# Optimization experiments

Measured on AMD Instinct MI355X. Metric: run time of the kernel, lower is better.

Reference implementation:

```python
import jax, jax.numpy as jnp
import numpy as np

IN_FEATURES = 4096
OUT_FEATURES = 1024
BATCH = 16384
WERR = 1.0
BERR = 1.0


def setup_inputs() -> dict:
    key = jax.random.key(0)
    kx, kw = jax.random.split(key)
    X = jax.random.normal(kx, (BATCH, IN_FEATURES), dtype=jnp.float32)
    # glorot_uniform init for W, zeros for bias (as in Keras layer)
    limit = np.sqrt(6.0 / (IN_FEATURES + OUT_FEATURES)).astype(np.float32)
    W = jax.random.uniform(kw, (IN_FEATURES, OUT_FEATURES), dtype=jnp.float32,
                           minval=-limit, maxval=limit)
    bias = jnp.zeros((1, OUT_FEATURES), dtype=jnp.float32)
    return {"X": X, "W": W, "bias": bias}


def reference(X, W, bias):
    # Binarize weights/bias with sign(), scaled by Werr/Berr, then dense matmul.
    Wb = jnp.sign(W) * WERR          # [in, out], values in {-1, 0, +1}
    bb = jnp.sign(bias) * BERR       # [1, out]
    Z = jnp.matmul(X, Wb) + bb       # [batch, out]
    return Z
```

## Files before the change

### kernel.cpp

```cpp
#include <hip/hip_runtime.h>

#define M_DIM 16384
#define N_DIM 1024
#define K_DIM 4096

#define BM 256
#define BN 256
#define BK 64
#define NT (K_DIM / BK)

typedef __attribute__((ext_vector_type(4))) float f32x4;
typedef __attribute__((ext_vector_type(8))) short bf16x8;
typedef __attribute__((ext_vector_type(8))) unsigned short u16x8;

static __device__ __forceinline__ short f2bf(float f) {
  union { __bf16 h; short s; } u;
  u.h = (__bf16)f;
  return u.s;
}

static __device__ __forceinline__ void load_lds16(const void* g, void* l) {
  __builtin_amdgcn_global_load_lds(
      (const __attribute__((address_space(1))) void*)g,
      (__attribute__((address_space(3))) void*)l, 16, 0, 0);
}

__global__ __launch_bounds__(256) void wsign_transpose(
    const float* __restrict__ W, unsigned short* __restrict__ WbT) {
  __shared__ unsigned short tile[64][72];
  const int t  = (int)threadIdx.x;
  const int k0 = (int)(blockIdx.x >> 4) * 64;
  const int n0 = (int)(blockIdx.x & 15) * 64;
#pragma unroll
  for (int p = 0; p < 4; ++p) {
    const int r = p * 16 + (t >> 4);
    const int c = (t & 15) * 4;
    const float* src = W + (size_t)(k0 + r) * N_DIM + n0 + c;
#pragma unroll
    for (int j = 0; j < 4; ++j) {
      const float w = src[j];
      tile[r][c + j] = (w > 0.f) ? (unsigned short)0x3F80u
                                 : ((w < 0.f) ? (unsigned short)0xBF80u
                                              : (unsigned short)0u);
    }
  }
  __syncthreads();
  const int n  = t >> 2;
  const int kg = (t & 3) * 16;
  u16x8 o0, o1;
#pragma unroll
  for (int j = 0; j < 8; ++j) o0[j] = tile[kg + j][n];
#pragma unroll
  for (int j = 0; j < 8; ++j) o1[j] = tile[kg + 8 + j][n];
  unsigned short* dst = WbT + (size_t)(n0 + n) * K_DIM + k0 + kg;
  *(u16x8*)dst       = o0;
  *(u16x8*)(dst + 8) = o1;
}

__global__ __launch_bounds__(512, 2) void gemm_p4(
    const float* __restrict__ X, const unsigned short* __restrict__ WbT,
    const float* __restrict__ bias, float* __restrict__ Z) {
  __shared__ __align__(16) unsigned short As[2][BM * BK];
  __shared__ __align__(16) unsigned short Bs[2][BN * BK];

  const int t   = (int)threadIdx.x;
  const int l   = t & 63;
  const int wid = t >> 6;
  const int wm  = wid >> 2;
  const int wn  = wid & 3;

  const int bid = (int)blockIdx.x;
  const int swz = (bid & 7) * 32 + (bid >> 3);
  const int m0  = (swz >> 2) * BM;
  const int n0  = (swz & 3) * BN;

  const int abase = (wm * 128 + (l & 15)) * BK;
  const int bbase = (wn * 64 + (l & 15)) * BK;
  const int axk0  = (((l >> 4) + 0) ^ (l & 7)) << 3;
  const int axk1  = (((l >> 4) + 4) ^ (l & 7)) << 3;

  const float* sA0 = X + (size_t)(m0 +   0 + (t >> 3)) * K_DIM + (t & 7) * 8;
  const float* sA1 = X + (size_t)(m0 +  64 + (t >> 3)) * K_DIM + (t & 7) * 8;
  const float* sA2 = X + (size_t)(m0 + 128 + (t >> 3)) * K_DIM + (t & 7) * 8;
  const float* sA3 = X + (size_t)(m0 + 192 + (t >> 3)) * K_DIM + (t & 7) * 8;
  const int adst = (t >> 3) * BK + (((t & 7) ^ ((t >> 3) & 7)) << 3);

  const unsigned short* b_src[4];
  int b_dst[4];
#pragma unroll
  for (int i = 0; i < 4; ++i) {
    const int c = i * 512 + t;
    const int n = c >> 3, gp = c & 7;
    b_src[i] = WbT + (size_t)(n0 + n) * K_DIM + (gp ^ (n & 7)) * 8;
    b_dst[i] = c * 8;
  }

  f32x4 acc[8][4] = {};
  f32x4 ar1[2][2], ar2[2][2];
  bf16x8 aF[2][4];
  bf16x8 bF0[2][2], bF1[2][2];

#define SB0 __builtin_amdgcn_sched_barrier(0)
#define BAR do { SB0; __builtin_amdgcn_s_barrier(); SB0; } while (0)
#define WVM(N) do { asm volatile("s_waitcnt vmcnt(" #N ")" ::: "memory"); SB0; } while (0)
#define WLG0 do { asm volatile("s_waitcnt lgkmcnt(0)" ::: "memory"); SB0; } while (0)

#define LD_A1(KT)                                                          \
  do { SB0;                                                                \
    ar1[0][0] = *(const f32x4*)(sA0 + (KT));                               \
    ar1[0][1] = *(const f32x4*)(sA0 + (KT) + 4);                           \
    ar1[1][0] = *(const f32x4*)(sA1 + (KT));                               \
    ar1[1][1] = *(const f32x4*)(sA1 + (KT) + 4); SB0;                      \
  } while (0)
#define LD_A2(KT)                                                          \
  do { SB0;                                                                \
    ar2[0][0] = *(const f32x4*)(sA2 + (KT));                               \
    ar2[0][1] = *(const f32x4*)(sA2 + (KT) + 4);                           \
    ar2[1][0] = *(const f32x4*)(sA3 + (KT));                               \
    ar2[1][1] = *(const f32x4*)(sA3 + (KT) + 4); SB0;                      \
  } while (0)
#define WR_A(AR, BUF, OFS)                                                 \
  do {                                                                     \
    _Pragma("unroll") for (int j = 0; j < 2; ++j) {                        \
      u16x8 v;                                                             \
      _Pragma("unroll") for (int q = 0; q < 4; ++q) {                      \
        v[q]     = (unsigned short)f2bf(AR[j][0][q]);                      \
        v[4 + q] = (unsigned short)f2bf(AR[j][1][q]);                      \
      }                                                                    \
      *(u16x8*)(&As[BUF][adst + (OFS) + j * 4096]) = v;                    \
    }                                                                      \
  } while (0)
#define DMA_B2(KT, BUF, I0)                                                \
  do { SB0;                                                                \
    _Pragma("unroll") for (int i = (I0); i < (I0) + 2; ++i)                \
      load_lds16(b_src[i] + (KT), &Bs[BUF][b_dst[i]]);                     \
    SB0;                                                                   \
  } while (0)
#define RD_A(MH, AB)                                                       \
  do { SB0;                                                                \
    _Pragma("unroll") for (int mi = 0; mi < 4; ++mi) {                     \
      aF[0][mi] = *(const bf16x8*)((AB) + abase + ((MH)*4 + mi) * 1024 + axk0); \
      aF[1][mi] = *(const bf16x8*)((AB) + abase + ((MH)*4 + mi) * 1024 + axk1); \
    } SB0;                                                                 \
  } while (0)
#define RD_B(DST, NH, BB)                                                  \
  do { SB0;                                                                \
    _Pragma("unroll") for (int nj = 0; nj < 2; ++nj) {                     \
      DST[0][nj] = *(const bf16x8*)((BB) + bbase + ((NH)*2 + nj) * 1024 + axk0); \
      DST[1][nj] = *(const bf16x8*)((BB) + bbase + ((NH)*2 + nj) * 1024 + axk1); \
    } SB0;                                                                 \
  } while (0)
#define Q(MH, NH, BF)                                                      \
  do { __builtin_amdgcn_s_setprio(1);                                      \
    _Pragma("unroll") for (int kk = 0; kk < 2; ++kk)                       \
      _Pragma("unroll") for (int mi = 0; mi < 4; ++mi)                     \
        _Pragma("unroll") for (int nj = 0; nj < 2; ++nj)                   \
          acc[(MH)*4 + mi][(NH)*2 + nj] =                                  \
              __builtin_amdgcn_mfma_f32_16x16x32_bf16(                     \
                  aF[kk][mi], BF[kk][nj], acc[(MH)*4 + mi][(NH)*2 + nj],   \
                  0, 0, 0);                                                \
    __builtin_amdgcn_s_setprio(0);                                         \
  } while (0)

  LD_A1(0); LD_A2(0);
  WVM(4); WR_A(ar1, 0, 0);
  WVM(0); WR_A(ar2, 0, 8192);
  DMA_B2(0, 0, 0); DMA_B2(0, 0, 2);
  LD_A1(BK); LD_A2(BK);
  WLG0;
  BAR;

  for (int tt = 0; tt < NT - 2; ++tt) {
    const int cur = tt & 1, nxt = cur ^ 1;
    const unsigned short* Ab = As[cur];
    const unsigned short* Bb = Bs[cur];
    const int kt1 = (tt + 1) * BK, kt2 = (tt + 2) * BK;
    WVM(8);
    RD_A(0, Ab);
    RD_B(bF0, 0, Bb);
    BAR; WLG0;
    Q(0, 0, bF0);
    BAR;
    WVM(4);
    WR_A(ar1, nxt, 0);
    RD_B(bF1, 1, Bb);
    DMA_B2(kt1, nxt, 0);
    BAR; WLG0;
    Q(0, 1, bF1);
    BAR;
    WVM(2);
    WR_A(ar2, nxt, 8192);
    RD_A(1, Ab);
    DMA_B2(kt1, nxt, 2);
    LD_A1(kt2);
    BAR; WLG0;
    Q(1, 1, bF1);
    BAR;
    LD_A2(kt2);
    Q(1, 0, bF0);
    BAR;
  }

  {
    const int cur = (NT - 2) & 1, nxt = cur ^ 1;
    const unsigned short* Ab = As[cur];
    const unsigned short* Bb = Bs[cur];
    const int kt1 = (NT - 1) * BK;
    WVM(8);
    RD_A(0, Ab);
    RD_B(bF0, 0, Bb);
    BAR; WLG0;
    Q(0, 0, bF0);
    BAR;
    WVM(4);
    WR_A(ar1, nxt, 0);
    RD_B(bF1, 1, Bb);
    DMA_B2(kt1, nxt, 0);
    BAR; WLG0;
    Q(0, 1, bF1);
    BAR;
    WVM(2);
    WR_A(ar2, nxt, 8192);
    RD_A(1, Ab);
    DMA_B2(kt1, nxt, 2);
    BAR; WLG0;
    Q(1, 1, bF1);
    BAR;
    Q(1, 0, bF0);
    BAR;
  }
  {
    const unsigned short* Ab = As[(NT - 1) & 1];
    const unsigned short* Bb = Bs[(NT - 1) & 1];
    WVM(0);
    RD_A(0, Ab);
    RD_B(bF0, 0, Bb);
    WLG0;
    Q(0, 0, bF0);
    RD_B(bF1, 1, Bb);
    WLG0;
    Q(0, 1, bF1);
    RD_A(1, Ab);
    WLG0;
    Q(1, 1, bF1);
    Q(1, 0, bF0);
  }

#pragma unroll
  for (int ni = 0; ni < 4; ++ni) {
    const int col = n0 + wn * 64 + ni * 16 + (l & 15);
    const float b  = bias[col];
    const float bs = (b > 0.f) ? 1.f : ((b < 0.f) ? -1.f : 0.f);
#pragma unroll
    for (int mi = 0; mi < 8; ++mi) {
      const int row = m0 + wm * 128 + mi * 16 + ((l >> 4) << 2);
#pragma unroll
      for (int j = 0; j < 4; ++j)
        Z[(size_t)(row + j) * N_DIM + col] = acc[mi][ni][j] + bs;
    }
  }
#undef SB0
#undef BAR
#undef WVM
#undef WLG0
#undef LD_A1
#undef LD_A2
#undef WR_A
#undef DMA_B2
#undef RD_A
#undef RD_B
#undef Q
}

__global__ __launch_bounds__(256) void naive_fb(
    const float* __restrict__ X, const float* __restrict__ W,
    const float* __restrict__ bias, float* __restrict__ Z) {
  const size_t id = (size_t)blockIdx.x * 256 + threadIdx.x;
  const int m = (int)(id >> 10), n = (int)(id & 1023);
  float acc = 0.f;
  for (int k = 0; k < K_DIM; ++k) {
    const float w = W[(size_t)k * N_DIM + n];
    const float s = (w > 0.f) ? 1.f : ((w < 0.f) ? -1.f : 0.f);
    acc += X[(size_t)m * K_DIM + k] * s;
  }
  const float b = bias[n];
  Z[id] = acc + ((b > 0.f) ? 1.f : ((b < 0.f) ? -1.f : 0.f));
}

extern "C" void kernel_launch(void* const* d_in, const int* in_sizes, int n_in,
                              void* d_out, int out_size, void* d_ws, size_t ws_size,
                              hipStream_t stream) {
  const float* X    = (const float*)d_in[0];
  const float* W    = (const float*)d_in[1];
  const float* bias = (const float*)d_in[2];
  float* Z = (float*)d_out;

  const size_t needW = (size_t)N_DIM * K_DIM * sizeof(unsigned short);
  if (ws_size >= needW) {
    unsigned short* WbT = (unsigned short*)d_ws;
    wsign_transpose<<<dim3((K_DIM / 64) * (N_DIM / 64)), dim3(256), 0, stream>>>(W, WbT);
    gemm_p4<<<dim3((M_DIM / BM) * (N_DIM / BN)), dim3(512), 0, stream>>>(X, WbT, bias, Z);
  } else {
    naive_fb<<<dim3((size_t)M_DIM * N_DIM / 256), dim3(256), 0, stream>>>(X, W, bias, Z);
  }
}
```

Before: 187.1 us.

## Restructure GEMM inner loop into k-slice phases with 4x4 MFMA blocks

```diff
diff --git a/kernel.cpp b/kernel.cpp
--- a/kernel.cpp
+++ b/kernel.cpp
@@ -57,7 +57,7 @@
   *(u16x8*)(dst + 8) = o1;
 }
 
-__global__ __launch_bounds__(512, 2) void gemm_p4(
+__global__ __launch_bounds__(512, 2) void gemm_kk(
     const float* __restrict__ X, const unsigned short* __restrict__ WbT,
     const float* __restrict__ bias, float* __restrict__ Z) {
   __shared__ __align__(16) unsigned short As[2][BM * BK];
@@ -96,38 +96,35 @@
   }
 
   f32x4 acc[8][4] = {};
-  f32x4 ar1[2][2], ar2[2][2];
-  bf16x8 aF[2][4];
-  bf16x8 bF0[2][2], bF1[2][2];
+  f32x4 ar[4][2];
+  bf16x8 aR[4];
+  bf16x8 bR[4];
 
 #define SB0 __builtin_amdgcn_sched_barrier(0)
 #define BAR do { SB0; __builtin_amdgcn_s_barrier(); SB0; } while (0)
 #define WVM(N) do { asm volatile("s_waitcnt vmcnt(" #N ")" ::: "memory"); SB0; } while (0)
 #define WLG0 do { asm volatile("s_waitcnt lgkmcnt(0)" ::: "memory"); SB0; } while (0)
 
-#define LD_A1(KT)                                                          \
+#define LD_A8(KT)                                                          \
   do { SB0;                                                                \
-    ar1[0][0] = *(const f32x4*)(sA0 + (KT));                               \
-    ar1[0][1] = *(const f32x4*)(sA0 + (KT) + 4);                           \
-    ar1[1][0] = *(const f32x4*)(sA1 + (KT));                               \
-    ar1[1][1] = *(const f32x4*)(sA1 + (KT) + 4); SB0;                      \
-  } while (0)
-#define LD_A2(KT)                                                          \
-  do { SB0;                                                                \
-    ar2[0][0] = *(const f32x4*)(sA2 + (KT));                               \
-    ar2[0][1] = *(const f32x4*)(sA2 + (KT) + 4);                           \
-    ar2[1][0] = *(const f32x4*)(sA3 + (KT));                               \
-    ar2[1][1] = *(const f32x4*)(sA3 + (KT) + 4); SB0;                      \
-  } while (0)
-#define WR_A(AR, BUF, OFS)                                                 \
+    ar[0][0] = *(const f32x4*)(sA0 + (KT));                                \
+    ar[0][1] = *(const f32x4*)(sA0 + (KT) + 4);                            \
+    ar[1][0] = *(const f32x4*)(sA1 + (KT));                                \
+    ar[1][1] = *(const f32x4*)(sA1 + (KT) + 4);                            \
+    ar[2][0] = *(const f32x4*)(sA2 + (KT));                                \
+    ar[2][1] = *(const f32x4*)(sA2 + (KT) + 4);                            \
+    ar[3][0] = *(const f32x4*)(sA3 + (KT));                                \
+    ar[3][1] = *(const f32x4*)(sA3 + (KT) + 4); SB0;                       \
+  } while (0)
+#define WR_AH(BUF, H)                                                      \
   do {                                                                     \
-    _Pragma("unroll") for (int j = 0; j < 2; ++j) {                        \
+    _Pragma("unroll") for (int j = 2 * (H); j < 2 * (H) + 2; ++j) {        \
       u16x8 v;                                                             \
       _Pragma("unroll") for (int q = 0; q < 4; ++q) {                      \
-        v[q]     = (unsigned short)f2bf(AR[j][0][q]);                      \
-        v[4 + q] = (unsigned short)f2bf(AR[j][1][q]);                      \
+        v[q]     = (unsigned short)f2bf(ar[j][0][q]);                      \
+        v[4 + q] = (unsigned short)f2bf(ar[j][1][q]);                      \
       }                                                                    \
-      *(u16x8*)(&As[BUF][adst + (OFS) + j * 4096]) = v;                    \
+      *(u16x8*)(&As[BUF][adst + j * 4096]) = v;                            \
     }                                                                      \
   } while (0)
 #define DMA_B2(KT, BUF, I0)                                                \
@@ -136,68 +133,67 @@
       load_lds16(b_src[i] + (KT), &Bs[BUF][b_dst[i]]);                     \
     SB0;                                                                   \
   } while (0)
-#define RD_A(MH, AB)                                                       \
+#define RD_A4(KK, MIG, AB)                                                 \
   do { SB0;                                                                \
-    _Pragma("unroll") for (int mi = 0; mi < 4; ++mi) {                     \
-      aF[0][mi] = *(const bf16x8*)((AB) + abase + ((MH)*4 + mi) * 1024 + axk0); \
-      aF[1][mi] = *(const bf16x8*)((AB) + abase + ((MH)*4 + mi) * 1024 + axk1); \
-    } SB0;                                                                 \
-  } while (0)
-#define RD_B(DST, NH, BB)                                                  \
+    _Pragma("unroll") for (int mi = 0; mi < 4; ++mi)                       \
+      aR[mi] = *(const bf16x8*)((AB) + abase + ((MIG)*4 + mi) * 1024 +     \
+                                ((KK) ? axk1 : axk0));                     \
+    SB0;                                                                   \
+  } while (0)
+#define RD_B4(KK, BB)                                                      \
   do { SB0;                                                                \
-    _Pragma("unroll") for (int nj = 0; nj < 2; ++nj) {                     \
-      DST[0][nj] = *(const bf16x8*)((BB) + bbase + ((NH)*2 + nj) * 1024 + axk0); \
-      DST[1][nj] = *(const bf16x8*)((BB) + bbase + ((NH)*2 + nj) * 1024 + axk1); \
-    } SB0;                                                                 \
-  } while (0)
-#define Q(MH, NH, BF)                                                      \
+    _Pragma("unroll") for (int nj = 0; nj < 4; ++nj)                       \
+      bR[nj] = *(const bf16x8*)((BB) + bbase + nj * 1024 +                 \
+                                ((KK) ? axk1 : axk0));                     \
+    SB0;                                                                   \
+  } while (0)
+#define MFMA16(MIG)                                                        \
   do { __builtin_amdgcn_s_setprio(1);                                      \
-    _Pragma("unroll") for (int kk = 0; kk < 2; ++kk)                       \
-      _Pragma("unroll") for (int mi = 0; mi < 4; ++mi)                     \
-        _Pragma("unroll") for (int nj = 0; nj < 2; ++nj)                   \
-          acc[(MH)*4 + mi][(NH)*2 + nj] =                                  \
-              __builtin_amdgcn_mfma_f32_16x16x32_bf16(                     \
-                  aF[kk][mi], BF[kk][nj], acc[(MH)*4 + mi][(NH)*2 + nj],   \
-                  0, 0, 0);                                                \
+    _Pragma("unroll") for (int mi = 0; mi < 4; ++mi)                       \
+      _Pragma("unroll") for (int nj = 0; nj < 4; ++nj)                     \
+        acc[(MIG)*4 + mi][nj] = __builtin_amdgcn_mfma_f32_16x16x32_bf16(   \
+            aR[mi], bR[nj], acc[(MIG)*4 + mi][nj], 0, 0, 0);               \
     __builtin_amdgcn_s_setprio(0);                                         \
   } while (0)
 
-  LD_A1(0); LD_A2(0);
-  WVM(4); WR_A(ar1, 0, 0);
-  WVM(0); WR_A(ar2, 0, 8192);
+  LD_A8(0);
+  WVM(0);
+  WR_AH(0, 0); WR_AH(0, 1);
   DMA_B2(0, 0, 0); DMA_B2(0, 0, 2);
-  LD_A1(BK); LD_A2(BK);
+  LD_A8(BK);
+  WVM(8);
   WLG0;
   BAR;
 
-  for (int tt = 0; tt < NT - 2; ++tt) {
+  for (int tt = 0; tt <= NT - 3; ++tt) {
     const int cur = tt & 1, nxt = cur ^ 1;
     const unsigned short* Ab = As[cur];
     const unsigned short* Bb = Bs[cur];
     const int kt1 = (tt + 1) * BK, kt2 = (tt + 2) * BK;
+    RD_B4(0, Bb);
+    RD_A4(0, 0, Ab);
+    DMA_B2(kt1, nxt, 0);
+    BAR; WLG0;
+    MFMA16(0);
+    BAR;
+    RD_A4(0, 1, Ab);
+    DMA_B2(kt1, nxt, 2);
+    WVM(4);
+    WR_AH(nxt, 0);
+    BAR; WLG0;
+    MFMA16(1);
+    BAR;
+    RD_B4(1, Bb);
+    RD_A4(1, 0, Ab);
+    WR_AH(nxt, 1);
+    LD_A8(kt2);
+    BAR; WLG0;
+    MFMA16(0);
+    BAR;
+    RD_A4(1, 1, Ab);
     WVM(8);
-    RD_A(0, Ab);
-    RD_B(bF0, 0, Bb);
-    BAR; WLG0;
-    Q(0, 0, bF0);
-    BAR;
-    WVM(4);
-    WR_A(ar1, nxt, 0);
-    RD_B(bF1, 1, Bb);
-    DMA_B2(kt1, nxt, 0);
-    BAR; WLG0;
-    Q(0, 1, bF1);
-    BAR;
-    WVM(2);
-    WR_A(ar2, nxt, 8192);
-    RD_A(1, Ab);
-    DMA_B2(kt1, nxt, 2);
-    LD_A1(kt2);
-    BAR; WLG0;
-    Q(1, 1, bF1);
-    BAR;
-    LD_A2(kt2);
-    Q(1, 0, bF0);
+    BAR; WLG0;
+    MFMA16(1);
     BAR;
   }
 
@@ -206,44 +202,48 @@
     const unsigned short* Ab = As[cur];
     const unsigned short* Bb = Bs[cur];
     const int kt1 = (NT - 1) * BK;
-    WVM(8);
-    RD_A(0, Ab);
-    RD_B(bF0, 0, Bb);
-    BAR; WLG0;
-    Q(0, 0, bF0);
-    BAR;
+    RD_B4(0, Bb);
+    RD_A4(0, 0, Ab);
+    DMA_B2(kt1, nxt, 0);
+    BAR; WLG0;
+    MFMA16(0);
+    BAR;
+    RD_A4(0, 1, Ab);
+    DMA_B2(kt1, nxt, 2);
     WVM(4);
-    WR_A(ar1, nxt, 0);
-    RD_B(bF1, 1, Bb);
-    DMA_B2(kt1, nxt, 0);
-    BAR; WLG0;
-    Q(0, 1, bF1);
-    BAR;
-    WVM(2);
-    WR_A(ar2, nxt, 8192);
-    RD_A(1, Ab);
-    DMA_B2(kt1, nxt, 2);
-    BAR; WLG0;
-    Q(1, 1, bF1);
-    BAR;
-    Q(1, 0, bF0);
+    WR_AH(nxt, 0);
+    BAR; WLG0;
+    MFMA16(1);
+    BAR;
+    RD_B4(1, Bb);
+    RD_A4(1, 0, Ab);
+    WR_AH(nxt, 1);
+    BAR; WLG0;
+    MFMA16(0);
+    BAR;
+    RD_A4(1, 1, Ab);
+    WVM(0);
+    BAR; WLG0;
+    MFMA16(1);
     BAR;
   }
   {
     const unsigned short* Ab = As[(NT - 1) & 1];
     const unsigned short* Bb = Bs[(NT - 1) & 1];
-    WVM(0);
-    RD_A(0, Ab);
-    RD_B(bF0, 0, Bb);
+    RD_B4(0, Bb);
+    RD_A4(0, 0, Ab);
     WLG0;
-    Q(0, 0, bF0);
-    RD_B(bF1, 1, Bb);
+    MFMA16(0);
+    RD_A4(0, 1, Ab);
     WLG0;
-    Q(0, 1, bF1);
-    RD_A(1, Ab);
+    MFMA16(1);
+    RD_B4(1, Bb);
+    RD_A4(1, 0, Ab);
     WLG0;
-    Q(1, 1, bF1);
-    Q(1, 0, bF0);
+    MFMA16(0);
+    RD_A4(1, 1, Ab);
+    WLG0;
+    MFMA16(1);
   }
 
 #pragma unroll
@@ -263,13 +263,12 @@
 #undef BAR
 #undef WVM
 #undef WLG0
-#undef LD_A1
-#undef LD_A2
-#undef WR_A
+#undef LD_A8
+#undef WR_AH
 #undef DMA_B2
-#undef RD_A
-#undef RD_B
-#undef Q
+#undef RD_A4
+#undef RD_B4
+#undef MFMA16
 }
 
 __global__ __launch_bounds__(256) void naive_fb(
@@ -299,7 +298,7 @@
   if (ws_size >= needW) {
     unsigned short* WbT = (unsigned short*)d_ws;
     wsign_transpose<<<dim3((K_DIM / 64) * (N_DIM / 64)), dim3(256), 0, stream>>>(W, WbT);
-    gemm_p4<<<dim3((M_DIM / BM) * (N_DIM / BN)), dim3(512), 0, stream>>>(X, WbT, bias, Z);
+    gemm_kk<<<dim3((M_DIM / BM) * (N_DIM / BN)), dim3(512), 0, stream>>>(X, WbT, bias, Z);
   } else {
     naive_fb<<<dim3((size_t)M_DIM * N_DIM / 256), dim3(256), 0, stream>>>(X, W, bias, Z);
   }
```

New measurement: 177.6 us. -5.0%, faster.
